# Optimization experiments

Hardware: AMD Instinct MI355X
Metric: run time of the kernel (lower is better)

Reference implementation:

```python
import jax, jax.numpy as jnp
import numpy as np

EMBED_DIM = 768
NUM_HEADS = 12
HEAD_DIM = EMBED_DIM // NUM_HEADS
EPS = 1e-5  # nn.LayerNorm default


def setup_inputs() -> dict:
    key = jax.random.key(0)
    ks = jax.random.split(key, 7)
    D = EMBED_DIM
    s1 = 1.0 / np.sqrt(D)
    x = jax.random.normal(ks[0], (2, 2048, D), dtype=jnp.float32)
    # LayerNorm params
    gamma = jnp.ones((D,), jnp.float32)
    beta = jnp.zeros((D,), jnp.float32)
    # QKV projection (linear1): weight [3D, D], bias [3D]
    w1 = jax.random.uniform(ks[1], (3 * D, D), jnp.float32, -s1, s1)
    b1 = jax.random.uniform(ks[2], (3 * D,), jnp.float32, -s1, s1)
    # Output projection (linear2[0]): weight [D, D], bias [D]
    w2 = jax.random.uniform(ks[3], (D, D), jnp.float32, -s1, s1)
    b2 = jax.random.uniform(ks[4], (D,), jnp.float32, -s1, s1)
    return {"x": x, "gamma": gamma, "beta": beta, "w1": w1, "b1": b1, "w2": w2, "b2": b2}


def _layernorm(x, gamma, beta):
    mu = jnp.mean(x, axis=-1, keepdims=True)
    var = jnp.mean(jnp.square(x - mu), axis=-1, keepdims=True)
    return (x - mu) * jax.lax.rsqrt(var + EPS) * gamma + beta


def reference(x, gamma, beta, w1, b1, w2, b2) -> jnp.ndarray:
    B, L, D = x.shape
    H, Dh = NUM_HEADS, HEAD_DIM
    residual = x
    h = _layernorm(x, gamma, beta)
    qkv = h @ w1.T + b1  # [B, L, 3D]
    q, k, v = jnp.split(qkv, 3, axis=-1)
    # 'b n (h d) -> b h n d'
    q = q.reshape(B, L, H, Dh).transpose(0, 2, 1, 3)
    k = k.reshape(B, L, H, Dh).transpose(0, 2, 1, 3)
    v = v.reshape(B, L, H, Dh).transpose(0, 2, 1, 3)
    scores = jnp.einsum("bhqd,bhkd->bhqk", q, k) / jnp.sqrt(jnp.float32(Dh))
    attn = jax.nn.softmax(scores, axis=-1)  # dropout is identity in eval mode
    out = jnp.einsum("bhqk,bhkd->bhqd", attn, v)  # [B, H, L, Dh]
    out = out.transpose(0, 2, 1, 3).reshape(B, L, D)
    out = out @ w2.T + b2  # dropout identity in eval
    return residual + out
```

## Files before the change

kernel.cpp:

```cpp
#include <hip/hip_runtime.h>


#define DEV __device__ __forceinline__

typedef __attribute__((ext_vector_type(4))) float f32x4;
typedef __attribute__((ext_vector_type(8))) short s16x8;
typedef __attribute__((ext_vector_type(2))) int i32x2;

constexpr int Bb   = 2;
constexpr int Ll   = 2048;
constexpr int Dd   = 768;
constexpr int Hh   = 12;
constexpr int Dh   = 64;
constexpr int Mrows = Bb * Ll;
constexpr int N1   = 3 * Dd;

DEV unsigned short f2bf(float f) {
  union { float f; unsigned u; } v; v.f = f;
  unsigned r = v.u + 0x7fffu + ((v.u >> 16) & 1u);
  return (unsigned short)(r >> 16);
}

DEV void gload_lds16(const void* g, void* l) {
  __builtin_amdgcn_global_load_lds((const __attribute__((address_space(1))) unsigned int*)g,
                                   (__attribute__((address_space(3))) unsigned int*)l,
                                   16, 0, 0);
}

DEV f32x4 mfma16(s16x8 a, s16x8 b, f32x4 c) {
  return __builtin_amdgcn_mfma_f32_16x16x32_bf16(a, b, c, 0, 0, 0);
}

DEV float fexp2(float x) { float r; asm("v_exp_f32 %0, %1" : "=v"(r) : "v"(x)); return r; }
DEV float frcp(float x)  { float r; asm("v_rcp_f32 %0, %1" : "=v"(r) : "v"(x)); return r; }

DEV float redmax64(float x) {
  x = fmaxf(x, __shfl_xor(x, 16, 64));
  float a = x, b = x;
  asm volatile("v_permlane32_swap_b32 %0, %1" : "+v"(a), "+v"(b));
  return fmaxf(a, b);
}
DEV float redsum64(float x) {
  x += __shfl_xor(x, 16, 64);
  float a = x, b = x;
  asm volatile("v_permlane32_swap_b32 %0, %1" : "+v"(a), "+v"(b));
  return a + b;
}

DEV void ln_body(int row, int t, const float* __restrict__ x,
                 const float* __restrict__ gamma, const float* __restrict__ beta,
                 short* __restrict__ hbuf, float* red) {
  const float* xr = x + (size_t)row * Dd;
  float v0 = xr[t], v1 = xr[t + 256], v2 = xr[t + 512];
  float s = v0 + v1 + v2;
  float q = v0 * v0 + v1 * v1 + v2 * v2;
#pragma unroll
  for (int off = 32; off; off >>= 1) {
    s += __shfl_xor(s, off, 64);
    q += __shfl_xor(q, off, 64);
  }
  const int w = t >> 6, lane = t & 63;
  if (lane == 0) { red[w] = s; red[4 + w] = q; }
  __syncthreads();
  s = red[0] + red[1] + red[2] + red[3];
  q = red[4] + red[5] + red[6] + red[7];
  const float mean = s * (1.f / Dd);
  const float var  = q * (1.f / Dd) - mean * mean;
  const float rstd = rsqrtf(var + 1e-5f);
  short* hr = hbuf + (size_t)row * Dd;
  hr[t]       = (short)f2bf((v0 - mean) * rstd * gamma[t]       + beta[t]);
  hr[t + 256] = (short)f2bf((v1 - mean) * rstd * gamma[t + 256] + beta[t + 256]);
  hr[t + 512] = (short)f2bf((v2 - mean) * rstd * gamma[t + 512] + beta[t + 512]);
}

constexpr int W1E = N1 * Dd;
constexpr int W2E = Dd * Dd;

__global__ __launch_bounds__(256) void ln_kernel(const float* __restrict__ x,
                                                 const float* __restrict__ gamma,
                                                 const float* __restrict__ beta,
                                                 short* __restrict__ hbuf) {
  __shared__ float red[8];
  ln_body(blockIdx.x, threadIdx.x, x, gamma, beta, hbuf, red);
}

__global__ __launch_bounds__(256) void cvt_kernel(const float* __restrict__ w1,
                                                  const float* __restrict__ w2,
                                                  short* __restrict__ w1b,
                                                  short* __restrict__ w2b) {
  int i = blockIdx.x * 256 + threadIdx.x;
  const int stride = gridDim.x * 256;
  for (; i < W1E + W2E; i += stride) {
    if (i < W1E) w1b[i] = (short)f2bf(w1[i]);
    else         w2b[i - W1E] = (short)f2bf(w2[i - W1E]);
  }
}

__global__ __launch_bounds__(256) void prep_kernel(const float* __restrict__ x,
                                                   const float* __restrict__ gamma,
                                                   const float* __restrict__ beta,
                                                   short* __restrict__ hbuf,
                                                   const float* __restrict__ w1,
                                                   const float* __restrict__ w2,
                                                   short* __restrict__ w1b,
                                                   short* __restrict__ w2b) {
  __shared__ float red[8];
  if (blockIdx.x < (unsigned)Mrows) {
    ln_body(blockIdx.x, threadIdx.x, x, gamma, beta, hbuf, red);
  } else {
    int i = (blockIdx.x - Mrows) * 256 + threadIdx.x;
    for (; i < W1E + W2E; i += 1024 * 256) {
      if (i < W1E) w1b[i] = (short)f2bf(w1[i]);
      else         w2b[i - W1E] = (short)f2bf(w2[i - W1E]);
    }
  }
}

DEV unsigned xcd_swz(unsigned f, unsigned nwg) {
  if ((nwg & 7u) != 0u) return f;
  return (f & 7u) * (nwg >> 3) + (f >> 3);
}

template <int EPI, int WSRC>
__global__ __launch_bounds__(256) void gemm_bt(const short* __restrict__ A,
                                               const void* __restrict__ Wp,
                                               const float* __restrict__ bias,
                                               const float* __restrict__ resid,
                                               void* __restrict__ outp,
                                               int N, int K) {
  __shared__ __align__(16) short As[2][128 * 64];
  __shared__ __align__(16) short Ws[2][128 * 64];
  const int tid  = threadIdx.x;
  const int lane = tid & 63, wid = tid >> 6;
  const int wr = wid >> 1, wc = wid & 1;
  const int g = lane >> 4, li = lane & 15;
  const unsigned o = xcd_swz(blockIdx.y * gridDim.x + blockIdx.x,
                             gridDim.x * gridDim.y);
  const int brow = (int)(o / gridDim.x) * 128, bcol = (int)(o % gridDim.x) * 128;

  f32x4 acc[4][4];
#pragma unroll
  for (int m = 0; m < 4; ++m)
#pragma unroll
    for (int n = 0; n < 4; ++n)
#pragma unroll
      for (int r = 0; r < 4; ++r) acc[m][n][r] = 0.f;

  if constexpr (WSRC == 0) {
    const short* W = (const short*)Wp;
    const int nt = K >> 6;
    auto stage = [&](int t, int buf) {
      const int ko = t << 6;
#pragma unroll
      for (int i = 0; i < 4; ++i) {
        const int idx = i * 256 + tid;
        const int r = idx >> 3, c = idx & 7;
        const int cs = c ^ (r & 7);
        gload_lds16(A + (size_t)(brow + r) * K + ko + cs * 8,
                    (char*)&As[buf][0] + idx * 16);
        gload_lds16(W + (size_t)(bcol + r) * K + ko + cs * 8,
                    (char*)&Ws[buf][0] + idx * 16);
      }
    };
    stage(0, 0);
    stage(1, 1);
    for (int it = 0; it < nt; ++it) {
      const int cur = it & 1;
      if (it + 1 < nt) asm volatile("s_waitcnt vmcnt(8)" ::: "memory");
      else             asm volatile("s_waitcnt vmcnt(0)" ::: "memory");
      __builtin_amdgcn_s_barrier();
      __builtin_amdgcn_sched_barrier(0);
#pragma unroll
      for (int kk = 0; kk < 2; ++kk) {
        s16x8 af[4], bf[4];
#pragma unroll
        for (int m = 0; m < 4; ++m) {
          const int row = wr * 64 + m * 16 + li;
          af[m] = *(const s16x8*)&As[cur][row * 64 + (((kk * 4 + g) ^ (li & 7)) & 7) * 8];
        }
#pragma unroll
        for (int n = 0; n < 4; ++n) {
          const int row = wc * 64 + n * 16 + li;
          bf[n] = *(const s16x8*)&Ws[cur][row * 64 + (((kk * 4 + g) ^ (li & 7)) & 7) * 8];
        }
#pragma unroll
        for (int m = 0; m < 4; ++m)
#pragma unroll
          for (int n = 0; n < 4; ++n)
            acc[m][n] = mfma16(af[m], bf[n], acc[m][n]);
      }
      __builtin_amdgcn_s_barrier();
      if (it + 2 < nt) stage(it + 2, cur);
    }
  } else {
    const float* W = (const float*)Wp;
    for (int kt = 0; kt < K; kt += 64) {
#pragma unroll
      for (int i = 0; i < 4; ++i) {
        const int idx = i * 256 + tid;
        const int r = idx >> 3, c = idx & 7;
        const int cs = c ^ (r & 7);
        gload_lds16(A + (size_t)(brow + r) * K + kt + cs * 8,
                    (char*)&As[0][0] + idx * 16);
      }
#pragma unroll
      for (int i = 0; i < 4; ++i) {
        const int idx = i * 256 + tid;
        const int r = idx >> 3, c = idx & 7;
        const float* wp = W + (size_t)(bcol + r) * K + kt + c * 8;
        const f32x4 lo = *(const f32x4*)wp;
        const f32x4 hi = *(const f32x4*)(wp + 4);
        s16x8 oo;
#pragma unroll
        for (int j = 0; j < 4; ++j) {
          oo[j]     = (short)f2bf(lo[j]);
          oo[4 + j] = (short)f2bf(hi[j]);
        }
        *(s16x8*)((char*)&Ws[0][0] + (size_t)(r * 8 + (c ^ (r & 7))) * 16) = oo;
      }
      __syncthreads();
#pragma unroll
      for (int kk = 0; kk < 2; ++kk) {
        s16x8 af[4], bf[4];
#pragma unroll
        for (int m = 0; m < 4; ++m) {
          const int row = wr * 64 + m * 16 + li;
          af[m] = *(const s16x8*)&As[0][row * 64 + (((kk * 4 + g) ^ (li & 7)) & 7) * 8];
        }
#pragma unroll
        for (int n = 0; n < 4; ++n) {
          const int row = wc * 64 + n * 16 + li;
          bf[n] = *(const s16x8*)&Ws[0][row * 64 + (((kk * 4 + g) ^ (li & 7)) & 7) * 8];
        }
#pragma unroll
        for (int m = 0; m < 4; ++m)
#pragma unroll
          for (int n = 0; n < 4; ++n)
            acc[m][n] = mfma16(af[m], bf[n], acc[m][n]);
      }
      __syncthreads();
    }
  }

#pragma unroll
  for (int m = 0; m < 4; ++m) {
#pragma unroll
    for (int n = 0; n < 4; ++n) {
      const int col = bcol + wc * 64 + n * 16 + li;
      const float bv = bias[col];
#pragma unroll
      for (int r = 0; r < 4; ++r) {
        const int row = brow + wr * 64 + m * 16 + g * 4 + r;
        const float v = acc[m][n][r] + bv;
        if (EPI == 0) {
          ((short*)outp)[(size_t)row * N + col] = (short)f2bf(v);
        } else {
          const size_t o2 = (size_t)row * N + col;
          ((float*)outp)[o2] = v + resid[o2];
        }
      }
    }
  }
}

#define TRRD(dst, addr, OFF)                                                   \
  asm volatile("ds_read_b64_tr_b16 %0, %1 offset:" #OFF                        \
               : "=v"(dst) : "v"(addr))

__global__ __launch_bounds__(256) void attn_kernel(const short* __restrict__ qkv,
                                                   short* __restrict__ obuf) {
  __shared__ __align__(16) short Ks[2][64 * 64];
  __shared__ __align__(16) short Vt[2][64 * 64];
  __shared__ __align__(16) short Ps[4][16 * 64];
  const int tid  = threadIdx.x;
  const int lane = tid & 63, w = tid >> 6;
  const int g = lane >> 4, li = lane & 15;
  const unsigned o = xcd_swz(blockIdx.y * 32u + blockIdx.x, gridDim.x * gridDim.y);
  const int bh = (int)(o >> 5);
  const int b = bh / Hh, h = bh % Hh;
  const size_t rowbase = (size_t)b * Ll * N1;
  const int q0 = (int)(o & 31u) * 64 + w * 16;
  constexpr float kScale = 0.125f * 1.44269504f;
  constexpr float kThrRaw = 8.f / kScale;
  constexpr int KVSTRIDE = 64 * N1;

  s16x8 qf[2];
#pragma unroll
  for (int ks = 0; ks < 2; ++ks)
    qf[ks] = *(const s16x8*)(qkv + rowbase + (size_t)(q0 + li) * N1 +
                             h * Dh + ks * 32 + g * 8);

  f32x4 oa[4];
  float m_ = -1e30f, l_ = 0.f;
#pragma unroll
  for (int dn = 0; dn < 4; ++dn)
#pragma unroll
    for (int r = 0; r < 4; ++r) oa[dn][r] = 0.f;

  constexpr int NT = Ll / 64;

  const int ia = tid, ib = 256 + tid;
  const int ra = ia >> 3, ca = ia & 7, rb = ib >> 3, cb = ib & 7;
  const short* kpa = qkv + rowbase + Dd + h * Dh + (size_t)ra * N1 + (ca ^ (ra & 7)) * 8;
  const short* kpb = qkv + rowbase + Dd + h * Dh + (size_t)rb * N1 + (cb ^ (rb & 7)) * 8;
  const int Ta = ia >> 3, Tb = ib >> 3;
  const short* vpa = qkv + rowbase + 2 * Dd + h * Dh +
                     (size_t)((Ta & 15) * 4 + (ca >> 1)) * N1 + (Ta >> 4) * 16 + (ia & 1) * 8;
  const short* vpb = qkv + rowbase + 2 * Dd + h * Dh +
                     (size_t)((Tb & 15) * 4 + (cb >> 1)) * N1 + (Tb >> 4) * 16 + (ib & 1) * 8;
  char* KsB = (char*)&Ks[0][0];
  char* VtB = (char*)&Vt[0][0];
  const int dsta = ia * 16, dstb = ib * 16;

  int koff[4][2];
#pragma unroll
  for (int n = 0; n < 4; ++n) {
    koff[n][0] = ((n * 16 + li) * 64 + ((g ^ (li & 7)) & 7) * 8) * 2;
    koff[n][1] = ((n * 16 + li) * 64 + (((4 + g) ^ (li & 7)) & 7) * 8) * 2;
  }
  int pwoff[4], proff[2];
#pragma unroll
  for (int n = 0; n < 4; ++n)
    pwoff[n] = li * 128 + (((2 * n + (g >> 1)) ^ (li & 7)) << 4) + 8 * (g & 1);
#pragma unroll
  for (int kk = 0; kk < 2; ++kk)
    proff[kk] = li * 128 + (((4 * kk + g) ^ (li & 7)) << 4);
  char* Pw = (char*)&Ps[w][0];
  const unsigned vlane = (unsigned)((lane >> 4) * 256 + (lane & 15) * 2);
  const unsigned vbase0 = (unsigned)(unsigned long long)(&Vt[0][0]) + vlane;

  auto stageK = [&](int buf) {
    const int bo = buf << 13;
    gload_lds16(kpa, KsB + bo + dsta);
    gload_lds16(kpb, KsB + bo + dstb);
    kpa += KVSTRIDE; kpb += KVSTRIDE;
  };
  auto stageV = [&](int buf) {
    const int bo = buf << 13;
    gload_lds16(vpa, VtB + bo + dsta);
    gload_lds16(vpb, VtB + bo + dstb);
    vpa += KVSTRIDE; vpb += KVSTRIDE;
  };

  stageK(0); stageV(0); stageK(1); stageV(1);
  asm volatile("s_waitcnt vmcnt(4)" ::: "memory");
  __builtin_amdgcn_s_barrier();
  __builtin_amdgcn_sched_barrier(0);

  f32x4 zA[4], zB[4];
#pragma unroll
  for (int n = 0; n < 4; ++n) {
    s16x8 kf0 = *(const s16x8*)(KsB + koff[n][0]);
    s16x8 kf1 = *(const s16x8*)(KsB + koff[n][1]);
    f32x4 z;
#pragma unroll
    for (int r = 0; r < 4; ++r) z[r] = 0.f;
    z = mfma16(kf0, qf[0], z);
    z = mfma16(kf1, qf[1], z);
    zA[n] = z;
  }

  auto body = [&](int kt, int cur, f32x4 (&zC)[4], f32x4 (&zN)[4]) {
    const int curo = cur << 13;
    const int nxto = (cur ^ 1) << 13;
    if (kt + 1 < NT) asm volatile("s_waitcnt vmcnt(2)" ::: "memory");
    else             asm volatile("s_waitcnt vmcnt(0)" ::: "memory");
    __builtin_amdgcn_s_barrier();
    __builtin_amdgcn_sched_barrier(0);

    if (kt + 2 < NT) stageK(cur);

    if (kt + 1 < NT) {
      __builtin_amdgcn_s_setprio(1);
#pragma unroll
      for (int n = 0; n < 4; ++n) {
        s16x8 kf0 = *(const s16x8*)(KsB + nxto + koff[n][0]);
        s16x8 kf1 = *(const s16x8*)(KsB + nxto + koff[n][1]);
        f32x4 z;
#pragma unroll
        for (int r = 0; r < 4; ++r) z[r] = 0.f;
        z = mfma16(kf0, qf[0], z);
        z = mfma16(kf1, qf[1], z);
        zN[n] = z;
      }
      __builtin_amdgcn_s_setprio(0);
    }

    const float t0 = fmaxf(fmaxf(zC[0][0], zC[0][1]), zC[0][2]);
    const float t1 = fmaxf(fmaxf(zC[0][3], zC[1][0]), zC[1][1]);
    const float t2 = fmaxf(fmaxf(zC[1][2], zC[1][3]), zC[2][0]);
    const float t3 = fmaxf(fmaxf(zC[2][1], zC[2][2]), zC[2][3]);
    const float t4 = fmaxf(fmaxf(zC[3][0], zC[3][1]), zC[3][2]);
    const float mloc = fmaxf(fmaxf(fmaxf(fmaxf(t0, t1), t2), fmaxf(t3, t4)), zC[3][3]);
    if (!__all(mloc - m_ <= kThrRaw)) {
      const float mxr = redmax64(mloc);
      const float mnew = fmaxf(m_, mxr);
      const float sc = fexp2((m_ - mnew) * kScale);
      float scq[4];
#pragma unroll
      for (int r = 0; r < 4; ++r)
        scq[r] = __shfl(sc, (lane & 48) + ((lane & 48) >> 2) + r, 64);
#pragma unroll
      for (int dn = 0; dn < 4; ++dn)
#pragma unroll
        for (int r = 0; r < 4; ++r) oa[dn][r] *= scq[r];
      l_ *= sc;
      m_ = mnew;
    }
    const float msc = m_ * kScale;
#pragma unroll
    for (int n = 0; n < 4; ++n)
#pragma unroll
      for (int r = 0; r < 4; ++r) {
        const float p = fexp2(fmaf(zC[n][r], kScale, -msc));
        zC[n][r] = p;
        l_ += p;
      }

#pragma unroll
    for (int n = 0; n < 4; ++n) {
      unsigned u0, u1;
      asm("v_cvt_pk_bf16_f32 %0, %1, %2" : "=v"(u0) : "v"(zC[n][0]), "v"(zC[n][1]));
      asm("v_cvt_pk_bf16_f32 %0, %1, %2" : "=v"(u1) : "v"(zC[n][2]), "v"(zC[n][3]));
      i32x2 pv; pv[0] = (int)u0; pv[1] = (int)u1;
      *(i32x2*)(Pw + pwoff[n]) = pv;
    }

    s16x8 pf[2];
#pragma unroll
    for (int kk = 0; kk < 2; ++kk)
      pf[kk] = *(const s16x8*)(Pw + proff[kk]);

    union VU { long l[2]; s16x8 v; };
    VU vu[4][2];
    {
      const unsigned vaddr = vbase0 + (unsigned)curo;
      TRRD(vu[0][0].l[0], vaddr, 0);    TRRD(vu[0][0].l[1], vaddr, 128);
      TRRD(vu[0][1].l[0], vaddr, 1024); TRRD(vu[0][1].l[1], vaddr, 1152);
      TRRD(vu[1][0].l[0], vaddr, 2048); TRRD(vu[1][0].l[1], vaddr, 2176);
      TRRD(vu[1][1].l[0], vaddr, 3072); TRRD(vu[1][1].l[1], vaddr, 3200);
      TRRD(vu[2][0].l[0], vaddr, 4096); TRRD(vu[2][0].l[1], vaddr, 4224);
      TRRD(vu[2][1].l[0], vaddr, 5120); TRRD(vu[2][1].l[1], vaddr, 5248);
      TRRD(vu[3][0].l[0], vaddr, 6144); TRRD(vu[3][0].l[1], vaddr, 6272);
      TRRD(vu[3][1].l[0], vaddr, 7168); TRRD(vu[3][1].l[1], vaddr, 7296);
    }
    asm volatile("s_waitcnt lgkmcnt(0)" ::: "memory");
    __builtin_amdgcn_sched_barrier(0);

    __builtin_amdgcn_s_setprio(1);
#pragma unroll
    for (int dn = 0; dn < 4; ++dn) {
      oa[dn] = mfma16(pf[0], vu[dn][0].v, oa[dn]);
      oa[dn] = mfma16(pf[1], vu[dn][1].v, oa[dn]);
    }
    __builtin_amdgcn_s_setprio(0);

    __builtin_amdgcn_s_barrier();
    if (kt + 2 < NT) stageV(cur);
  };

  for (int g2 = 0; g2 < NT / 2; ++g2) {
    body(2 * g2,     0, zA, zB);
    body(2 * g2 + 1, 1, zB, zA);
  }

  l_ = redsum64(l_);
  {
#pragma unroll
    for (int r = 0; r < 4; ++r) {
      const float lq = __shfl(l_, (lane & 48) + ((lane & 48) >> 2) + r, 64);
      const float inv = frcp(lq);
      const int row = b * Ll + q0 + g * 4 + r;
#pragma unroll
      for (int dn = 0; dn < 4; ++dn)
        obuf[(size_t)row * Dd + h * Dh + dn * 16 + li] =
            (short)f2bf(oa[dn][r] * inv);
    }
  }
}

extern "C" void kernel_launch(void* const* d_in, const int* in_sizes, int n_in,
                              void* d_out, int out_size, void* d_ws, size_t ws_size,
                              hipStream_t stream) {
  const float* x     = (const float*)d_in[0];
  const float* gamma = (const float*)d_in[1];
  const float* beta  = (const float*)d_in[2];
  const float* w1    = (const float*)d_in[3];
  const float* b1    = (const float*)d_in[4];
  const float* w2    = (const float*)d_in[5];
  const float* b2    = (const float*)d_in[6];
  float* out = (float*)d_out;
  char* ws = (char*)d_ws;

  if (ws_size >= 29884416) {
    short* qkvb = (short*)(ws);
    short* hb   = (short*)(ws + 18874368);
    short* w1b  = (short*)(ws + 25165824);
    short* w2b  = (short*)(ws + 28704768);
    prep_kernel<<<dim3(Mrows + 1024), dim3(256), 0, stream>>>(
        x, gamma, beta, hb, w1, w2, w1b, w2b);
    gemm_bt<0, 0><<<dim3(N1 / 128, Mrows / 128), dim3(256), 0, stream>>>(
        hb, w1b, b1, nullptr, (void*)qkvb, N1, Dd);
    attn_kernel<<<dim3(Ll / 64, Bb * Hh), dim3(256), 0, stream>>>(qkvb, hb);
    gemm_bt<1, 0><<<dim3(Dd / 128, Mrows / 128), dim3(256), 0, stream>>>(
        hb, w2b, b2, x, (void*)out, Dd, Dd);
  } else if (ws_size >= 17301504) {
    short* qkvb = (short*)(ws);
    short* hb   = (short*)(ws + 9437184);
    short* w1b  = (short*)(ws + 12582912);
    short* w2b  = (short*)(ws + 16121856);
    cvt_kernel<<<dim3(1024), dim3(256), 0, stream>>>(w1, w2, w1b, w2b);
    for (int b = 0; b < Bb; ++b) {
      const size_t ro = (size_t)b * Ll * Dd;
      ln_kernel<<<dim3(Ll), dim3(256), 0, stream>>>(x + ro, gamma, beta, hb);
      gemm_bt<0, 0><<<dim3(N1 / 128, Ll / 128), dim3(256), 0, stream>>>(
          hb, w1b, b1, nullptr, (void*)qkvb, N1, Dd);
      attn_kernel<<<dim3(Ll / 64, Hh), dim3(256), 0, stream>>>(qkvb, hb);
      gemm_bt<1, 0><<<dim3(Dd / 128, Ll / 128), dim3(256), 0, stream>>>(
          hb, w2b, b2, x + ro, (void*)(out + ro), Dd, Dd);
    }
  } else {
    short* qkvb = (short*)(ws);
    short* hb   = (short*)(ws + 9437184);
    for (int b = 0; b < Bb; ++b) {
      const size_t ro = (size_t)b * Ll * Dd;
      ln_kernel<<<dim3(Ll), dim3(256), 0, stream>>>(x + ro, gamma, beta, hb);
      gemm_bt<0, 1><<<dim3(N1 / 128, Ll / 128), dim3(256), 0, stream>>>(
          hb, w1, b1, nullptr, (void*)qkvb, N1, Dd);
      attn_kernel<<<dim3(Ll / 64, Hh), dim3(256), 0, stream>>>(qkvb, hb);
      gemm_bt<1, 1><<<dim3(Dd / 128, Ll / 128), dim3(256), 0, stream>>>(
          hb, w2, b2, x + ro, (void*)(out + ro), Dd, Dd);
    }
  }
}
```

Measured before the change: 106.2 us.

## Process two 16-row query tiles per wave in attention kernel

```diff
diff --git a/kernel.cpp b/kernel.cpp
--- a/kernel.cpp
+++ b/kernel.cpp
@@ -271,31 +271,37 @@
                                                    short* __restrict__ obuf) {
   __shared__ __align__(16) short Ks[2][64 * 64];
   __shared__ __align__(16) short Vt[2][64 * 64];
-  __shared__ __align__(16) short Ps[4][16 * 64];
+  __shared__ __align__(16) short Ps[4][32 * 64];
   const int tid  = threadIdx.x;
   const int lane = tid & 63, w = tid >> 6;
   const int g = lane >> 4, li = lane & 15;
-  const unsigned o = xcd_swz(blockIdx.y * 32u + blockIdx.x, gridDim.x * gridDim.y);
-  const int bh = (int)(o >> 5);
+  const unsigned o = xcd_swz(blockIdx.y * gridDim.x + blockIdx.x,
+                             gridDim.x * gridDim.y);
+  const int bh = (int)(o / gridDim.x);
   const int b = bh / Hh, h = bh % Hh;
   const size_t rowbase = (size_t)b * Ll * N1;
-  const int q0 = (int)(o & 31u) * 64 + w * 16;
+  const int q0 = (int)(o % gridDim.x) * 128 + w * 32;
   constexpr float kScale = 0.125f * 1.44269504f;
   constexpr float kThrRaw = 8.f / kScale;
   constexpr int KVSTRIDE = 64 * N1;
 
-  s16x8 qf[2];
-#pragma unroll
-  for (int ks = 0; ks < 2; ++ks)
-    qf[ks] = *(const s16x8*)(qkv + rowbase + (size_t)(q0 + li) * N1 +
-                             h * Dh + ks * 32 + g * 8);
-
-  f32x4 oa[4];
-  float m_ = -1e30f, l_ = 0.f;
-#pragma unroll
-  for (int dn = 0; dn < 4; ++dn)
-#pragma unroll
-    for (int r = 0; r < 4; ++r) oa[dn][r] = 0.f;
+  s16x8 qf[2][2];
+#pragma unroll
+  for (int mq = 0; mq < 2; ++mq)
+#pragma unroll
+    for (int ks = 0; ks < 2; ++ks)
+      qf[mq][ks] = *(const s16x8*)(qkv + rowbase + (size_t)(q0 + mq * 16 + li) * N1 +
+                                   h * Dh + ks * 32 + g * 8);
+
+  f32x4 oa[2][4];
+  float m_[2] = {-1e30f, -1e30f};
+  float l_[2] = {0.f, 0.f};
+#pragma unroll
+  for (int mq = 0; mq < 2; ++mq)
+#pragma unroll
+    for (int dn = 0; dn < 4; ++dn)
+#pragma unroll
+      for (int r = 0; r < 4; ++r) oa[mq][dn][r] = 0.f;
 
   constexpr int NT = Ll / 64;
 
@@ -318,13 +324,15 @@
     koff[n][0] = ((n * 16 + li) * 64 + ((g ^ (li & 7)) & 7) * 8) * 2;
     koff[n][1] = ((n * 16 + li) * 64 + (((4 + g) ^ (li & 7)) & 7) * 8) * 2;
   }
-  int pwoff[4], proff[2];
+  int psw[4], prw[2], pwbase[2];
 #pragma unroll
   for (int n = 0; n < 4; ++n)
-    pwoff[n] = li * 128 + (((2 * n + (g >> 1)) ^ (li & 7)) << 4) + 8 * (g & 1);
+    psw[n] = (((2 * n + (g >> 1)) ^ (li & 7)) << 4) + 8 * (g & 1);
 #pragma unroll
   for (int kk = 0; kk < 2; ++kk)
-    proff[kk] = li * 128 + (((4 * kk + g) ^ (li & 7)) << 4);
+    prw[kk] = ((4 * kk + g) ^ (li & 7)) << 4;
+  pwbase[0] = li * 128;
+  pwbase[1] = (16 + li) * 128;
   char* Pw = (char*)&Ps[w][0];
   const unsigned vlane = (unsigned)((lane >> 4) * 256 + (lane & 15) * 2);
   const unsigned vbase0 = (unsigned)(unsigned long long)(&Vt[0][0]) + vlane;
@@ -347,20 +355,23 @@
   __builtin_amdgcn_s_barrier();
   __builtin_amdgcn_sched_barrier(0);
 
-  f32x4 zA[4], zB[4];
+  f32x4 zA[2][4], zB[2][4];
 #pragma unroll
   for (int n = 0; n < 4; ++n) {
     s16x8 kf0 = *(const s16x8*)(KsB + koff[n][0]);
     s16x8 kf1 = *(const s16x8*)(KsB + koff[n][1]);
-    f32x4 z;
-#pragma unroll
-    for (int r = 0; r < 4; ++r) z[r] = 0.f;
-    z = mfma16(kf0, qf[0], z);
-    z = mfma16(kf1, qf[1], z);
-    zA[n] = z;
-  }
-
-  auto body = [&](int kt, int cur, f32x4 (&zC)[4], f32x4 (&zN)[4]) {
+#pragma unroll
+    for (int mq = 0; mq < 2; ++mq) {
+      f32x4 z;
+#pragma unroll
+      for (int r = 0; r < 4; ++r) z[r] = 0.f;
+      z = mfma16(kf0, qf[mq][0], z);
+      z = mfma16(kf1, qf[mq][1], z);
+      zA[mq][n] = z;
+    }
+  }
+
+  auto body = [&](int kt, int cur, f32x4 (&zC)[2][4], f32x4 (&zN)[2][4]) {
     const int curo = cur << 13;
     const int nxto = (cur ^ 1) << 13;
     if (kt + 1 < NT) asm volatile("s_waitcnt vmcnt(2)" ::: "memory");
@@ -376,60 +387,71 @@
       for (int n = 0; n < 4; ++n) {
         s16x8 kf0 = *(const s16x8*)(KsB + nxto + koff[n][0]);
         s16x8 kf1 = *(const s16x8*)(KsB + nxto + koff[n][1]);
-        f32x4 z;
-#pragma unroll
-        for (int r = 0; r < 4; ++r) z[r] = 0.f;
-        z = mfma16(kf0, qf[0], z);
-        z = mfma16(kf1, qf[1], z);
-        zN[n] = z;
+#pragma unroll
+        for (int mq = 0; mq < 2; ++mq) {
+          f32x4 z;
+#pragma unroll
+          for (int r = 0; r < 4; ++r) z[r] = 0.f;
+          z = mfma16(kf0, qf[mq][0], z);
+          z = mfma16(kf1, qf[mq][1], z);
+          zN[mq][n] = z;
+        }
       }
       __builtin_amdgcn_s_setprio(0);
     }
 
-    const float t0 = fmaxf(fmaxf(zC[0][0], zC[0][1]), zC[0][2]);
-    const float t1 = fmaxf(fmaxf(zC[0][3], zC[1][0]), zC[1][1]);
-    const float t2 = fmaxf(fmaxf(zC[1][2], zC[1][3]), zC[2][0]);
-    const float t3 = fmaxf(fmaxf(zC[2][1], zC[2][2]), zC[2][3]);
-    const float t4 = fmaxf(fmaxf(zC[3][0], zC[3][1]), zC[3][2]);
-    const float mloc = fmaxf(fmaxf(fmaxf(fmaxf(t0, t1), t2), fmaxf(t3, t4)), zC[3][3]);
-    if (!__all(mloc - m_ <= kThrRaw)) {
-      const float mxr = redmax64(mloc);
-      const float mnew = fmaxf(m_, mxr);
-      const float sc = fexp2((m_ - mnew) * kScale);
-      float scq[4];
-#pragma unroll
-      for (int r = 0; r < 4; ++r)
-        scq[r] = __shfl(sc, (lane & 48) + ((lane & 48) >> 2) + r, 64);
-#pragma unroll
-      for (int dn = 0; dn < 4; ++dn)
-#pragma unroll
-        for (int r = 0; r < 4; ++r) oa[dn][r] *= scq[r];
-      l_ *= sc;
-      m_ = mnew;
-    }
-    const float msc = m_ * kScale;
-#pragma unroll
-    for (int n = 0; n < 4; ++n)
-#pragma unroll
-      for (int r = 0; r < 4; ++r) {
-        const float p = fexp2(fmaf(zC[n][r], kScale, -msc));
-        zC[n][r] = p;
-        l_ += p;
-      }
-
-#pragma unroll
-    for (int n = 0; n < 4; ++n) {
-      unsigned u0, u1;
-      asm("v_cvt_pk_bf16_f32 %0, %1, %2" : "=v"(u0) : "v"(zC[n][0]), "v"(zC[n][1]));
-      asm("v_cvt_pk_bf16_f32 %0, %1, %2" : "=v"(u1) : "v"(zC[n][2]), "v"(zC[n][3]));
-      i32x2 pv; pv[0] = (int)u0; pv[1] = (int)u1;
-      *(i32x2*)(Pw + pwoff[n]) = pv;
-    }
-
-    s16x8 pf[2];
-#pragma unroll
-    for (int kk = 0; kk < 2; ++kk)
-      pf[kk] = *(const s16x8*)(Pw + proff[kk]);
+#pragma unroll
+    for (int mq = 0; mq < 2; ++mq) {
+      const float t0 = fmaxf(fmaxf(zC[mq][0][0], zC[mq][0][1]), zC[mq][0][2]);
+      const float t1 = fmaxf(fmaxf(zC[mq][0][3], zC[mq][1][0]), zC[mq][1][1]);
+      const float t2 = fmaxf(fmaxf(zC[mq][1][2], zC[mq][1][3]), zC[mq][2][0]);
+      const float t3 = fmaxf(fmaxf(zC[mq][2][1], zC[mq][2][2]), zC[mq][2][3]);
+      const float t4 = fmaxf(fmaxf(zC[mq][3][0], zC[mq][3][1]), zC[mq][3][2]);
+      const float mloc = fmaxf(fmaxf(fmaxf(fmaxf(t0, t1), t2), fmaxf(t3, t4)),
+                               zC[mq][3][3]);
+      if (!__all(mloc - m_[mq] <= kThrRaw)) {
+        const float mxr = redmax64(mloc);
+        const float mnew = fmaxf(m_[mq], mxr);
+        const float sc = fexp2((m_[mq] - mnew) * kScale);
+        float scq[4];
+#pragma unroll
+        for (int r = 0; r < 4; ++r)
+          scq[r] = __shfl(sc, (lane & 48) + ((lane & 48) >> 2) + r, 64);
+#pragma unroll
+        for (int dn = 0; dn < 4; ++dn)
+#pragma unroll
+          for (int r = 0; r < 4; ++r) oa[mq][dn][r] *= scq[r];
+        l_[mq] *= sc;
+        m_[mq] = mnew;
+      }
+      const float msc = m_[mq] * kScale;
+#pragma unroll
+      for (int n = 0; n < 4; ++n)
+#pragma unroll
+        for (int r = 0; r < 4; ++r) {
+          const float p = fexp2(fmaf(zC[mq][n][r], kScale, -msc));
+          zC[mq][n][r] = p;
+          l_[mq] += p;
+        }
+    }
+
+#pragma unroll
+    for (int mq = 0; mq < 2; ++mq)
+#pragma unroll
+      for (int n = 0; n < 4; ++n) {
+        unsigned u0, u1;
+        asm("v_cvt_pk_bf16_f32 %0, %1, %2" : "=v"(u0) : "v"(zC[mq][n][0]), "v"(zC[mq][n][1]));
+        asm("v_cvt_pk_bf16_f32 %0, %1, %2" : "=v"(u1) : "v"(zC[mq][n][2]), "v"(zC[mq][n][3]));
+        i32x2 pv; pv[0] = (int)u0; pv[1] = (int)u1;
+        *(i32x2*)(Pw + pwbase[mq] + psw[n]) = pv;
+      }
+
+    s16x8 pf[2][2];
+#pragma unroll
+    for (int mq = 0; mq < 2; ++mq)
+#pragma unroll
+      for (int kk = 0; kk < 2; ++kk)
+        pf[mq][kk] = *(const s16x8*)(Pw + pwbase[mq] + prw[kk]);
 
     union VU { long l[2]; s16x8 v; };
     VU vu[4][2];
@@ -449,10 +471,12 @@
 
     __builtin_amdgcn_s_setprio(1);
 #pragma unroll
-    for (int dn = 0; dn < 4; ++dn) {
-      oa[dn] = mfma16(pf[0], vu[dn][0].v, oa[dn]);
-      oa[dn] = mfma16(pf[1], vu[dn][1].v, oa[dn]);
-    }
+    for (int mq = 0; mq < 2; ++mq)
+#pragma unroll
+      for (int dn = 0; dn < 4; ++dn) {
+        oa[mq][dn] = mfma16(pf[mq][0], vu[dn][0].v, oa[mq][dn]);
+        oa[mq][dn] = mfma16(pf[mq][1], vu[dn][1].v, oa[mq][dn]);
+      }
     __builtin_amdgcn_s_setprio(0);
 
     __builtin_amdgcn_s_barrier();
@@ -464,17 +488,18 @@
     body(2 * g2 + 1, 1, zB, zA);
   }
 
-  l_ = redsum64(l_);
-  {
+#pragma unroll
+  for (int mq = 0; mq < 2; ++mq) {
+    const float lsum = redsum64(l_[mq]);
 #pragma unroll
     for (int r = 0; r < 4; ++r) {
-      const float lq = __shfl(l_, (lane & 48) + ((lane & 48) >> 2) + r, 64);
+      const float lq = __shfl(lsum, (lane & 48) + ((lane & 48) >> 2) + r, 64);
       const float inv = frcp(lq);
-      const int row = b * Ll + q0 + g * 4 + r;
+      const int row = b * Ll + q0 + mq * 16 + g * 4 + r;
 #pragma unroll
       for (int dn = 0; dn < 4; ++dn)
         obuf[(size_t)row * Dd + h * Dh + dn * 16 + li] =
-            (short)f2bf(oa[dn][r] * inv);
+            (short)f2bf(oa[mq][dn][r] * inv);
     }
   }
 }
@@ -501,7 +526,7 @@
         x, gamma, beta, hb, w1, w2, w1b, w2b);
     gemm_bt<0, 0><<<dim3(N1 / 128, Mrows / 128), dim3(256), 0, stream>>>(
         hb, w1b, b1, nullptr, (void*)qkvb, N1, Dd);
-    attn_kernel<<<dim3(Ll / 64, Bb * Hh), dim3(256), 0, stream>>>(qkvb, hb);
+    attn_kernel<<<dim3(Ll / 128, Bb * Hh), dim3(256), 0, stream>>>(qkvb, hb);
     gemm_bt<1, 0><<<dim3(Dd / 128, Mrows / 128), dim3(256), 0, stream>>>(
         hb, w2b, b2, x, (void*)out, Dd, Dd);
   } else if (ws_size >= 17301504) {
@@ -515,7 +540,7 @@
       ln_kernel<<<dim3(Ll), dim3(256), 0, stream>>>(x + ro, gamma, beta, hb);
       gemm_bt<0, 0><<<dim3(N1 / 128, Ll / 128), dim3(256), 0, stream>>>(
           hb, w1b, b1, nullptr, (void*)qkvb, N1, Dd);
-      attn_kernel<<<dim3(Ll / 64, Hh), dim3(256), 0, stream>>>(qkvb, hb);
+      attn_kernel<<<dim3(Ll / 128, Hh), dim3(256), 0, stream>>>(qkvb, hb);
       gemm_bt<1, 0><<<dim3(Dd / 128, Ll / 128), dim3(256), 0, stream>>>(
           hb, w2b, b2, x + ro, (void*)(out + ro), Dd, Dd);
     }
@@ -527,7 +552,7 @@
       ln_kernel<<<dim3(Ll), dim3(256), 0, stream>>>(x + ro, gamma, beta, hb);
       gemm_bt<0, 1><<<dim3(N1 / 128, Ll / 128), dim3(256), 0, stream>>>(
           hb, w1, b1, nullptr, (void*)qkvb, N1, Dd);
-      attn_kernel<<<dim3(Ll / 64, Hh), dim3(256), 0, stream>>>(qkvb, hb);
+      attn_kernel<<<dim3(Ll / 128, Hh), dim3(256), 0, stream>>>(qkvb, hb);
       gemm_bt<1, 1><<<dim3(Dd / 128, Ll / 128), dim3(256), 0, stream>>>(
           hb, w2, b2, x + ro, (void*)(out + ro), Dd, Dd);
     }
```

Measured after the change: 114.0 us. 1.07x slower.
